# Optimization experiments

Hardware: AMD Instinct MI355X
Metric: run time of the kernel (lower is better)

The kernel has to match this reference:

```python
import jax, jax.numpy as jnp
import numpy as np

H = 4096
GROUP = 128          # per-token activation quant group, also weight block size
EPS = 1e-6
FP8_MAX = 448.0      # float8_e4m3fn max


def fp8_roundtrip(v):
    # simulate fp8 storage: cast to e4m3 and back to f32
    return v.astype(jnp.float8_e4m3fn).astype(jnp.float32)


def rms_norm(x, w):
    # vLLM RMSNorm: x * rsqrt(mean(x^2) + eps) * weight, computed in f32
    var = jnp.mean(x * x, axis=-1, keepdims=True)
    return x * jax.lax.rsqrt(var + EPS) * w


def fused_add_rms_norm(x, resid, w):
    z = x + resid
    return rms_norm(z, w), z


def group_quant_dequant(y):
    # dynamic per-token-group (1,128) symmetric fp8 quant, then dequant
    T, Hd = y.shape
    yg = y.reshape(T, Hd // GROUP, GROUP)
    amax = jnp.max(jnp.abs(yg), axis=-1, keepdims=True)
    scale = jnp.maximum(amax, 1e-12) / FP8_MAX
    q = fp8_roundtrip(yg / scale)
    return (q * scale).reshape(T, Hd)


def block_fp8_linear(y, wq, wscale):
    # W8A8 block fp8 GEMM: act quant (1,128) groups, weight (128,128) block scales.
    # Math-equivalent form: dequantize both operands, then GEMM.
    a = group_quant_dequant(y)                                   # [T, H]
    ws = jnp.repeat(jnp.repeat(wscale, GROUP, 0), GROUP, 1)       # [H, H]
    w = wq * ws                                                   # dequant weight
    return a @ w                                                  # [T, H]


def setup_inputs() -> dict:
    key = jax.random.key(0)
    ks = jax.random.split(key, 8)
    T = 16384
    x = jax.random.normal(ks[0], (T, H), dtype=jnp.float32)
    norm_w = jnp.ones((4, H), dtype=jnp.float32)
    # weights: rand in [0,1) stored as fp8 (simulated by roundtrip)
    w0 = fp8_roundtrip(jax.random.uniform(ks[1], (H, H), dtype=jnp.float32))
    w1 = fp8_roundtrip(jax.random.uniform(ks[2], (H, H), dtype=jnp.float32))
    w2 = fp8_roundtrip(jax.random.uniform(ks[3], (H, H), dtype=jnp.float32))
    sh = H // GROUP
    ws0 = jax.random.uniform(ks[4], (sh, sh), dtype=jnp.float32)
    ws1 = jax.random.uniform(ks[5], (sh, sh), dtype=jnp.float32)
    ws2 = jax.random.uniform(ks[6], (sh, sh), dtype=jnp.float32)
    return {"x": x, "norm_w": norm_w, "w0": w0, "w1": w1, "w2": w2,
            "ws0": ws0, "ws1": ws1, "ws2": ws2}


def reference(x, norm_w, w0, w1, w2, ws0, ws1, ws2):
    x = jax.nn.relu(x)
    resid = x
    y = rms_norm(x, norm_w[0])
    x2 = block_fp8_linear(y, w0, ws0)
    y2, resid = fused_add_rms_norm(x2, resid, norm_w[1])
    x3 = block_fp8_linear(y2, w1, ws1)
    y3, resid = fused_add_rms_norm(x3, resid, norm_w[2])
    x4 = block_fp8_linear(y3, w2, ws2)
    y4, resid = fused_add_rms_norm(x4, resid, norm_w[3])
    return y4
```

## Files before the change

### kernel.cpp

```cpp
#include <hip/hip_runtime.h>

typedef __attribute__((ext_vector_type(4))) float f32x4;
typedef __attribute__((ext_vector_type(4))) unsigned int u32x4;
typedef __attribute__((ext_vector_type(4))) int i32x4;
typedef __attribute__((ext_vector_type(8))) int i32x8;
typedef __attribute__((ext_vector_type(4))) unsigned short u16x4;
typedef unsigned char u8;
typedef unsigned short u16;
typedef unsigned int u32;

#define MBYTE (1024*1024)
#define TTOK 16384
#define HDIM 4096

__device__ __forceinline__ float f16tof32(u16 h) {
  _Float16 x;
  __builtin_memcpy(&x, &h, 2);
  return (float)x;
}
__device__ __forceinline__ u16 f32tof16(float f) {
  _Float16 x = (_Float16)f;
  u16 h;
  __builtin_memcpy(&h, &x, 2);
  return h;
}


__device__ __forceinline__ void gload_lds16(const void* g, void* l) {
  __builtin_amdgcn_global_load_lds((const __attribute__((address_space(1))) void*)g,
                                   (__attribute__((address_space(3))) void*)l, 16, 0, 0);
}

__global__ __launch_bounds__(256) void k_wconv(const float* __restrict__ w0,
                                               const float* __restrict__ w1,
                                               const float* __restrict__ w2,
                                               u8* __restrict__ out) {
  __shared__ float tl[64][68];
  const int tid = threadIdx.x;
  const int bn = blockIdx.x, bk = blockIdx.y, z = blockIdx.z;
  const float* W = (z == 0) ? w0 : (z == 1 ? w1 : w2);
  u8* o = out + (size_t)z * 16 * MBYTE;
#pragma unroll
  for (int it = 0; it < 4; ++it) {
    int idx = it * 256 + tid;
    int r = idx >> 4, c4 = idx & 15;
    f32x4 v = *(const f32x4*)(W + (size_t)(bk * 64 + r) * HDIM + bn * 64 + c4 * 4);
    *(f32x4*)&tl[r][c4 * 4] = v;
  }
  __syncthreads();
  {
    int n = tid >> 2, q4 = tid & 3;
    u32 dw[4];
#pragma unroll
    for (int d = 0; d < 4; ++d) {
      int k0 = (d >> 1) * 32 + q4 * 8 + (d & 1) * 4;
      int w = __builtin_amdgcn_cvt_pk_fp8_f32(tl[k0 + 0][n], tl[k0 + 1][n], 0, false);
      w = __builtin_amdgcn_cvt_pk_fp8_f32(tl[k0 + 2][n], tl[k0 + 3][n], w, true);
      dw[d] = (u32)w;
    }
    u32x4 pack = {dw[0], dw[1], dw[2], dw[3]};
    *(u32x4*)(o + (size_t)(bn * 64 + n) * HDIM + (bk >> 1) * 128 + (bk & 1) * 64 + q4 * 16) = pack;
  }
}

template <int MODE>
__global__ __launch_bounds__(256) void k_norm(const void* __restrict__ in_,
                                              u16* __restrict__ zout,
                                              const float* __restrict__ nw,
                                              u32* __restrict__ qout,
                                              float* __restrict__ asct,
                                              float* __restrict__ yout) {
  const int row = blockIdx.x, t = threadIdx.x;
  f32x4 v[4];
  float ss = 0.f;
#pragma unroll
  for (int j = 0; j < 4; ++j) {
    f32x4 a;
    if (MODE == 0) {
      const f32x4* inr = (const f32x4*)((const float*)in_ + (size_t)row * HDIM);
      a = inr[j * 256 + t];
      a.x = fmaxf(a.x, 0.f); a.y = fmaxf(a.y, 0.f);
      a.z = fmaxf(a.z, 0.f); a.w = fmaxf(a.w, 0.f);
      u16x4 rw;
      rw.x = f32tof16(a.x); rw.y = f32tof16(a.y);
      rw.z = f32tof16(a.z); rw.w = f32tof16(a.w);
      ((u16x4*)(zout + (size_t)row * HDIM))[j * 256 + t] = rw;
    } else {
      const u16x4* inr = (const u16x4*)((const u16*)in_ + (size_t)row * HDIM);
      u16x4 iv = inr[j * 256 + t];
      a.x = f16tof32(iv.x); a.y = f16tof32(iv.y);
      a.z = f16tof32(iv.z); a.w = f16tof32(iv.w);
    }
    v[j] = a;
    ss += a.x * a.x + a.y * a.y + a.z * a.z + a.w * a.w;
  }
#pragma unroll
  for (int m = 1; m <= 32; m <<= 1) ss += __shfl_xor(ss, m, 64);
  __shared__ float sred[4];
  if ((t & 63) == 0) sred[t >> 6] = ss;
  __syncthreads();
  float tot = sred[0] + sred[1] + sred[2] + sred[3];
  float rinv = rsqrtf(tot * (1.f / (float)HDIM) + 1e-6f);
#pragma unroll
  for (int j = 0; j < 4; ++j) {
    f32x4 nv = ((const f32x4*)nw)[j * 256 + t];
    f32x4 y;
    y.x = v[j].x * rinv * nv.x; y.y = v[j].y * rinv * nv.y;
    y.z = v[j].z * rinv * nv.z; y.w = v[j].w * rinv * nv.w;
    if (MODE == 2) {
      ((f32x4*)yout)[(size_t)row * 1024 + j * 256 + t] = y;
    } else {
      float am = fmaxf(fmaxf(fabsf(y.x), fabsf(y.y)), fmaxf(fabsf(y.z), fabsf(y.w)));
#pragma unroll
      for (int m = 1; m <= 16; m <<= 1) am = fmaxf(am, __shfl_xor(am, m, 64));
      am = fmaxf(am, 1e-12f);
      float scale = am / 448.f;
      float inv = 448.f / am;
      int d = __builtin_amdgcn_cvt_pk_fp8_f32(y.x * inv, y.y * inv, 0, false);
      d = __builtin_amdgcn_cvt_pk_fp8_f32(y.z * inv, y.w * inv, d, true);
      int k4 = j * 256 + t;
      int k4w = k4 & 31;
      int k4n = (k4 & ~31) | (((k4w >> 4) & 1) << 4) | (((k4w >> 1) & 3) << 2)
              | (((k4w >> 3) & 1) << 1) | (k4w & 1);
      qout[(size_t)row * 1024 + k4n] = (u32)d;
      if ((t & 31) == 0) asct[(size_t)(j * 8 + (t >> 5)) * TTOK + row] = scale;
    }
  }
}

__global__ __launch_bounds__(256, 2) void k_gemm(const u8* __restrict__ A,
                                                 const u8* __restrict__ B,
                                                 const float* __restrict__ aS,
                                                 const float* __restrict__ bS,
                                                 const u16* __restrict__ resid,
                                                 u16* __restrict__ Z) {
  __shared__ u8 Al[2][128 * 128];
  __shared__ u8 Bl[2][128 * 128];
  __shared__ float As[32 * 128];
  const int tid = threadIdx.x;
  const int lane = tid & 63, wave = tid >> 6;
  const int lin = blockIdx.x;
  const int xcd = lin & 7, tt = lin >> 3;
  const int sidx = tt >> 3, rr = tt & 7;
  const int sm = sidx >> 3, sn = sidx & 7;
  const int bm = xcd * 16 + sm * 2 + (rr >> 2);
  const int bn = sn * 4 + (rr & 3);
  const int brow = bm * 128, bcol = bn * 128;
  const int wrb = (wave >> 1) * 64, wcb = (wave & 1) * 64;
  const int r16 = lane & 15, q4 = lane >> 4;
  const int swz3 = r16 & 7;
  const int c0 = (q4 ^ swz3) << 4;
  const int c1 = ((4 + q4) ^ swz3) << 4;

  const int srow = tid >> 3;
  const int scol = (((tid & 7) ^ (srow & 7)) << 4);
  const u8* aP = A + (size_t)(brow + srow) * HDIM + scol;
  const u8* bP = B + (size_t)(bcol + srow) * HDIM + scol;
  const int ldst = tid * 16;

#define STAGE(c, kt) do {                                                       \
    _Pragma("unroll")                                                           \
    for (int i = 0; i < 4; ++i) {                                               \
      gload_lds16(aP + (size_t)(kt) * 128 + (size_t)i * 32 * HDIM,              \
                  &Al[c][i * 4096 + ldst]);                                     \
      gload_lds16(bP + (size_t)(kt) * 128 + (size_t)i * 32 * HDIM,              \
                  &Bl[c][i * 4096 + ldst]);                                     \
    }                                                                           \
  } while (0)

  const int kt_ = (tid >> 5);
  const int r_ = (tid & 31) * 4;
  float bv[4];
  f32x4 av[4];
#pragma unroll
  for (int i = 0; i < 4; ++i)
    bv[i] = bS[(i * 8 + kt_) * 32 + bn];
#pragma unroll
  for (int i = 0; i < 4; ++i)
    av[i] = *(const f32x4*)(aS + (size_t)(i * 8 + kt_) * TTOK + brow + r_);
  STAGE(0, 0);
  STAGE(1, 1);
  asm volatile("s_waitcnt vmcnt(16)" ::: "memory");
#pragma unroll
  for (int i = 0; i < 4; ++i) {
    av[i] *= bv[i];
    *(f32x4*)&As[i * 1024 + tid * 4] = av[i];
  }
  asm volatile("s_waitcnt lgkmcnt(0)" ::: "memory");

  f32x4 accm[4][4] = {};
  const f32x4 z4 = {0.f, 0.f, 0.f, 0.f};

#pragma unroll 1
  for (int kt = 0; kt < 32; ++kt) {
    const int cur = kt & 1;
    if (kt < 31) asm volatile("s_waitcnt vmcnt(8)" ::: "memory");
    else         asm volatile("s_waitcnt vmcnt(0)" ::: "memory");
    __builtin_amdgcn_s_barrier();
    __builtin_amdgcn_sched_barrier(0);

    i32x8 bfr[4];
#pragma unroll
    for (int n = 0; n < 4; ++n) {
      const u8* rp = &Bl[cur][(wcb + n * 16 + r16) * 128];
      i32x4 lo = *(const i32x4*)(rp + c0);
      i32x4 hi = *(const i32x4*)(rp + c1);
      bfr[n] = __builtin_shufflevector(lo, hi, 0, 1, 2, 3, 4, 5, 6, 7);
    }

#pragma unroll
    for (int m = 0; m < 4; ++m) {
      const u8* rp = &Al[cur][(wrb + m * 16 + r16) * 128];
      i32x4 lo = *(const i32x4*)(rp + c0);
      i32x4 hi = *(const i32x4*)(rp + c1);
      i32x8 afr = __builtin_shufflevector(lo, hi, 0, 1, 2, 3, 4, 5, 6, 7);
      const f32x4 s = *(const f32x4*)&As[kt * 128 + wrb + m * 16 + q4 * 4];
      f32x4 acc[4];
      __builtin_amdgcn_s_setprio(1);
#pragma unroll
      for (int n = 0; n < 4; ++n)
        acc[n] = __builtin_amdgcn_mfma_scale_f32_16x16x128_f8f6f4(
            afr, bfr[n], z4, 0, 0, 0, 0x7F7F7F7F, 0, 0x7F7F7F7F);
      __builtin_amdgcn_s_setprio(0);
#pragma unroll
      for (int n = 0; n < 4; ++n)
        accm[m][n] += acc[n] * s;
    }

    __builtin_amdgcn_sched_barrier(0);
    __builtin_amdgcn_s_barrier();
    if (kt < 30) STAGE(cur, kt + 2);
  }
#undef STAGE

#pragma unroll
  for (int m = 0; m < 4; ++m) {
#pragma unroll
    for (int r = 0; r < 4; ++r) {
      const size_t rowi = (size_t)(brow + wrb + m * 16 + q4 * 4 + r);
      const u16* Rp = resid + rowi * HDIM + bcol + wcb + r16;
      u16* Zp = Z + rowi * HDIM + bcol + wcb + r16;
#pragma unroll
      for (int n = 0; n < 4; ++n)
        Zp[n * 16] = f32tof16(accm[m][n][r] + f16tof32(Rp[n * 16]));
    }
  }
}

extern "C" void kernel_launch(void* const* d_in, const int* in_sizes, int n_in,
                              void* d_out, int out_size, void* d_ws, size_t ws_size,
                              hipStream_t stream) {
  const float* x  = (const float*)d_in[0];
  const float* nw = (const float*)d_in[1];
  const float* w0 = (const float*)d_in[2];
  const float* w1 = (const float*)d_in[3];
  const float* w2 = (const float*)d_in[4];
  const float* s0 = (const float*)d_in[5];
  const float* s1 = (const float*)d_in[6];
  const float* s2 = (const float*)d_in[7];
  float* out = (float*)d_out;
  char* ws = (char*)d_ws;

  u8*  wqt   = (u8*)ws;
  u32* q     = (u32*)(ws + (size_t)48 * MBYTE);
  float* asc = (float*)(ws + (size_t)112 * MBYTE);
  u16* zA    = (u16*)(ws + (size_t)114 * MBYTE);
  u16* zB    = (u16*)(ws + (size_t)242 * MBYTE);

  k_wconv<<<dim3(64, 64, 3), 256, 0, stream>>>(w0, w1, w2, wqt);

  k_norm<0><<<TTOK, 256, 0, stream>>>(x, zA, nw, q, asc, nullptr);
  k_gemm<<<4096, 256, 0, stream>>>((const u8*)q, wqt, asc, s0, zA, zB);

  k_norm<1><<<TTOK, 256, 0, stream>>>(zB, nullptr, nw + HDIM, q, asc, nullptr);
  k_gemm<<<4096, 256, 0, stream>>>((const u8*)q, wqt + (size_t)16 * MBYTE, asc, s1, zB, zA);

  k_norm<1><<<TTOK, 256, 0, stream>>>(zA, nullptr, nw + 2 * HDIM, q, asc, nullptr);
  k_gemm<<<4096, 256, 0, stream>>>((const u8*)q, wqt + (size_t)32 * MBYTE, asc, s2, zA, zB);

  k_norm<2><<<TTOK, 256, 0, stream>>>(zB, nullptr, nw + 3 * HDIM, nullptr, nullptr, out);
}
```

Measured before the change: 1.296 ms.

## Load GEMM A operand directly from global into registers, bypassing LDS

The A tile no longer goes through shared memory. Each wave loads its own MFMA A fragments straight from global memory into registers, one k-step ahead, while B stays double-buffered in LDS. The aim is to cut LDS traffic and LDS footprint, and to drop the LDS reads for A. The cost is that A global/L2 traffic doubles, since the two waves sharing rows each load them, and more VGPRs are used. The prefetch also has only a short distance in which to hide its latency.

```diff
diff --git a/kernel.cpp b/kernel.cpp
--- a/kernel.cpp
+++ b/kernel.cpp
@@ -134,7 +134,6 @@
                                                  const float* __restrict__ bS,
                                                  const u16* __restrict__ resid,
                                                  u16* __restrict__ Z) {
-  __shared__ u8 Al[2][128 * 128];
   __shared__ u8 Bl[2][128 * 128];
   __shared__ float As[32 * 128];
   const int tid = threadIdx.x;
@@ -154,17 +153,24 @@
 
   const int srow = tid >> 3;
   const int scol = (((tid & 7) ^ (srow & 7)) << 4);
-  const u8* aP = A + (size_t)(brow + srow) * HDIM + scol;
   const u8* bP = B + (size_t)(bcol + srow) * HDIM + scol;
   const int ldst = tid * 16;
 
-#define STAGE(c, kt) do {                                                       \
+#define BSTAGE(c, kt) do {                                                      \
     _Pragma("unroll")                                                           \
-    for (int i = 0; i < 4; ++i) {                                               \
-      gload_lds16(aP + (size_t)(kt) * 128 + (size_t)i * 32 * HDIM,              \
-                  &Al[c][i * 4096 + ldst]);                                     \
+    for (int i = 0; i < 4; ++i)                                                 \
       gload_lds16(bP + (size_t)(kt) * 128 + (size_t)i * 32 * HDIM,              \
                   &Bl[c][i * 4096 + ldst]);                                     \
+  } while (0)
+
+  const u8* aD = A + (size_t)(brow + wrb + r16) * HDIM + q4 * 16;
+
+#define APREF(kt) do {                                                          \
+    _Pragma("unroll")                                                           \
+    for (int m = 0; m < 4; ++m) {                                               \
+      const u8* p_ = aD + (size_t)m * 16 * HDIM + (size_t)(kt) * 128;           \
+      aA[2 * m]     = *(const i32x4*)(p_);                                      \
+      aA[2 * m + 1] = *(const i32x4*)(p_ + 64);                                 \
     }                                                                           \
   } while (0)
 
@@ -178,8 +184,10 @@
 #pragma unroll
   for (int i = 0; i < 4; ++i)
     av[i] = *(const f32x4*)(aS + (size_t)(i * 8 + kt_) * TTOK + brow + r_);
-  STAGE(0, 0);
-  STAGE(1, 1);
+  i32x4 aA[8];
+  BSTAGE(0, 0);
+  APREF(0);
+  BSTAGE(1, 1);
   asm volatile("s_waitcnt vmcnt(16)" ::: "memory");
 #pragma unroll
   for (int i = 0; i < 4; ++i) {
@@ -194,7 +202,7 @@
 #pragma unroll 1
   for (int kt = 0; kt < 32; ++kt) {
     const int cur = kt & 1;
-    if (kt < 31) asm volatile("s_waitcnt vmcnt(8)" ::: "memory");
+    if (kt < 31) asm volatile("s_waitcnt vmcnt(4)" ::: "memory");
     else         asm volatile("s_waitcnt vmcnt(0)" ::: "memory");
     __builtin_amdgcn_s_barrier();
     __builtin_amdgcn_sched_barrier(0);
@@ -210,10 +218,8 @@
 
 #pragma unroll
     for (int m = 0; m < 4; ++m) {
-      const u8* rp = &Al[cur][(wrb + m * 16 + r16) * 128];
-      i32x4 lo = *(const i32x4*)(rp + c0);
-      i32x4 hi = *(const i32x4*)(rp + c1);
-      i32x8 afr = __builtin_shufflevector(lo, hi, 0, 1, 2, 3, 4, 5, 6, 7);
+      i32x8 afr = __builtin_shufflevector(aA[2 * m], aA[2 * m + 1],
+                                          0, 1, 2, 3, 4, 5, 6, 7);
       const f32x4 s = *(const f32x4*)&As[kt * 128 + wrb + m * 16 + q4 * 4];
       f32x4 acc[4];
       __builtin_amdgcn_s_setprio(1);
@@ -227,11 +233,14 @@
         accm[m][n] += acc[n] * s;
     }
 
+    if (kt < 31) APREF(kt + 1);
+
     __builtin_amdgcn_sched_barrier(0);
     __builtin_amdgcn_s_barrier();
-    if (kt < 30) STAGE(cur, kt + 2);
-  }
-#undef STAGE
+    if (kt < 30) BSTAGE(cur, kt + 2);
+  }
+#undef BSTAGE
+#undef APREF
 
 #pragma unroll
   for (int m = 0; m < 4; ++m) {
```

New measurement: 2.043 ms. 57.7% more time.
